# Performance work log

Measured on AMD Instinct MI355X. Metric: run time of the kernel, lower is better.

Reference implementation:

```python
import jax, jax.numpy as jnp
import numpy as np
import jax.scipy.signal as jss

SX, SY, C, K = 256, 256, 3, 10
C0 = [0, 0, 0, 1, 1, 1, 2, 2, 2, 0]
C1 = [[0, 1, 2, 9], [3, 4, 5], [6, 7, 8]]
DD, DT, SIGMA = 5, 0.2, 0.65

_KX = jnp.array([[-1., 0., 1.], [-2., 0., 2.], [-1., 0., 1.]])
_KY = _KX.T


def _conv2(A, Kf):
    # zero-padded 'same' 2D true convolution, vmapped over channel axis
    return jax.vmap(lambda a: jss.convolve2d(a, Kf, mode='same'), in_axes=2, out_axes=2)(A)


def sobel(A):
    # (X, Y, c) -> (X, Y, 2, c): [sobel_y, sobel_x] stacked on axis 2 (FlowLenia convention)
    return jnp.concatenate([_conv2(A, _KY)[:, :, None, :], _conv2(A, _KX)[:, :, None, :]], axis=2)


def growth(U, m, s):
    # bell(U,m,s)*2 - 1
    return jnp.exp(-((U - m) / s) ** 2 / 2.) * 2. - 1.


def get_kernels_fft(R, r, a, w, b):
    # FlowLenia kernel construction: ring distance -> smooth cutoff * sum-of-bumps, normalized, fft2(fftshift)
    mid = SX // 2
    xs = jnp.arange(-mid, mid, dtype=jnp.float32)
    D = jnp.sqrt(xs[:, None] ** 2 + xs[None, :] ** 2)            # (X, Y)
    Dk = D[..., None] / ((R + 15.) * r)                          # (X, Y, k)
    ker = (b * jnp.exp(-(Dk[..., None] - a) ** 2 / w)).sum(-1)   # (X, Y, k)
    sig = 0.5 * (jnp.tanh(-(Dk - 1.) * 10. / 2.) + 1.)           # sigmoid(-(D-1)*10)
    Kk = sig * ker
    nK = Kk / Kk.sum(axis=(0, 1), keepdims=True)
    return jnp.fft.fft2(jnp.fft.fftshift(nK, axes=(0, 1)), axes=(0, 1))


def _rt_apply(A, F):
    # Reintegration tracking with 'wall' border: flow-driven mass redistribution over a (2dd+1)^2 neighborhood
    ii = jnp.arange(SX, dtype=jnp.float32)
    pos = jnp.stack(jnp.meshgrid(ii, ii, indexing='ij'), axis=-1) + 0.5   # (X, Y, 2) cell centers
    ma = DD - SIGMA                                   # max flow magnitude
    mu = pos[..., None] + jnp.clip(DT * F, -ma, ma)   # (X, Y, 2, C) target centers
    mu = jnp.clip(mu, SIGMA, SX - SIGMA)              # wall border
    offs = jnp.arange(-DD, DD + 1)
    gx, gy = jnp.meshgrid(offs, offs, indexing='ij')
    dxs, dys = gx.reshape(-1), gy.reshape(-1)
    clip_hi = min(1., 2. * SIGMA)

    def step(dx, dy):
        Ar = jnp.roll(A, (dx, dy), axis=(0, 1))
        mur = jnp.roll(mu, (dx, dy), axis=(0, 1))
        dpmu = jnp.abs(pos[..., None] - mur)                                  # (X, Y, 2, C)
        sz = 0.5 - dpmu + SIGMA
        area = jnp.prod(jnp.clip(sz, 0., clip_hi), axis=2) / (4. * SIGMA ** 2)  # (X, Y, C)
        return Ar * area

    return jax.vmap(step)(dxs, dys).sum(axis=0)


def setup_inputs() -> dict:
    key = jax.random.key(0)
    ks = jax.random.split(key, 9)
    A = jax.random.uniform(ks[0], (SX, SY, C), dtype=jnp.float32)
    R = jax.random.uniform(ks[1], (), minval=2.0, maxval=25.0)
    r = jax.random.uniform(ks[2], (K,), minval=0.2, maxval=1.0)
    m = jax.random.uniform(ks[3], (K,), minval=0.05, maxval=0.5)
    s = jax.random.uniform(ks[4], (K,), minval=0.001, maxval=0.18)
    h = jax.random.uniform(ks[5], (K,), minval=0.01, maxval=1.0)
    a = jax.random.uniform(ks[6], (K, 3), minval=0.0, maxval=1.0)
    b = jax.random.uniform(ks[7], (K, 3), minval=0.001, maxval=1.0)
    w = jax.random.uniform(ks[8], (K, 3), minval=0.01, maxval=0.5)
    return dict(A=A, R=R, r=r, m=m, s=s, h=h, a=a, b=b, w=w)


def reference(A, R, r, m, s, h, a, b, w):
    fK = get_kernels_fft(R, r, a, w, b)                       # (X, Y, k) complex
    fA = jnp.fft.fft2(A, axes=(0, 1))
    fAk = fA[:, :, jnp.array(C0)]                             # (X, Y, k)
    U = jnp.real(jnp.fft.ifft2(fK * fAk, axes=(0, 1)))        # (X, Y, k)
    U = growth(U, m, s) * h
    U = jnp.dstack([U[:, :, C1[c]].sum(axis=-1) for c in range(C)])  # (X, Y, C)
    nabla_U = sobel(U)                                        # (X, Y, 2, C)
    nabla_A = sobel(A.sum(axis=-1, keepdims=True))            # (X, Y, 2, 1)
    alpha = jnp.clip((A[:, :, None, :] / C) ** 2, 0., 1.)     # (X, Y, 1, C)
    F = nabla_U * (1. - alpha) - nabla_A * alpha              # (X, Y, 2, C)
    return _rt_apply(A, F)
```

## Files before the change

### kernel.cpp

```cpp
#include <hip/hip_runtime.h>

#define NPIX 65536

#define WS_APLANE 0
#define WS_ASUM   (3*NPIX)
#define WS_KOFF   (4*NPIX)
#define WS_MUX    (4*NPIX)
#define WS_MUY    (7*NPIX)
#define WS_UACC   (14*NPIX)
#define WS_ROWS   (24*NPIX)
#define WS_X1RE   (25*NPIX)
#define WS_X1IM   (38*NPIX)
#define WS_X2RE   (51*NPIX)
#define WS_X2IM   (64*NPIX)
#define WS_END    (77*NPIX)

__global__ void k_prep(const float* __restrict__ A,
                       const float* __restrict__ R_, const float* __restrict__ r_,
                       const float* __restrict__ a_, const float* __restrict__ b_,
                       const float* __restrict__ w_, float* __restrict__ ws) {
    int bid = blockIdx.x;
    int t = threadIdx.x;
    if (bid < 256) {
        int idx = bid * 256 + t;
        float a0 = A[idx*3+0], a1 = A[idx*3+1], a2 = A[idx*3+2];
        ws[WS_APLANE + idx]          = a0;
        ws[WS_APLANE + NPIX + idx]   = a1;
        ws[WS_APLANE + 2*NPIX + idx] = a2;
        ws[WS_ASUM + idx] = a0 + a1 + a2;
        return;
    }
    __shared__ float red[4];
    int bk = bid - 256;
    int k = bk >> 8;
    int i = bk & 255;
    int wid = t >> 6, lane = t & 63;
    float R = R_[0];
    float denom = (R + 15.0f) * r_[k];
    int di = i - 128, dj = t - 128;
    float D  = sqrtf((float)(di*di + dj*dj));
    float Dk = D / denom;
    float v = 0.0f;
    if (Dk <= 3.0f) {
        float ker = 0.0f;
        #pragma unroll
        for (int tt = 0; tt < 3; ++tt) {
            float d = Dk - a_[k*3+tt];
            ker += b_[k*3+tt] * expf(-((d*d) / w_[k*3+tt]));
        }
        float sig = 1.0f / (1.0f + expf(10.0f * (Dk - 1.0f)));
        v = sig * ker;
    }
    int iw = (i + 128) & 255;
    int jw = (t + 128) & 255;
    ws[WS_KOFF + k*NPIX + iw*256 + jw] = v;
    float s = v;
    #pragma unroll
    for (int off = 32; off; off >>= 1) s += __shfl_xor(s, off);
    if (lane == 0) red[wid] = s;
    __syncthreads();
    if (t == 0) ws[WS_ROWS + k*256 + i] = red[0] + red[1] + red[2] + red[3];
}

__device__ __forceinline__ void fft256_core(float* __restrict__ re, float* __restrict__ im,
                                            const float* __restrict__ twr,
                                            const float* __restrict__ twi, int lane) {
    #pragma unroll
    for (int s = 1; s <= 8; ++s) {
        int h = 1 << (s - 1);
        #pragma unroll
        for (int b = 0; b < 2; ++b) {
            int idx = b*64 + lane;
            int pos = idx & (h - 1);
            int g   = idx >> (s - 1);
            int i0 = (g << s) + pos;
            int i1 = i0 + h;
            int tj = pos << (8 - s);
            float wr = twr[tj], wi = twi[tj];
            float xr = re[i1], xi = im[i1];
            float br = fmaf(xr, wr, -xi*wi);
            float bi = fmaf(xr, wi,  xi*wr);
            float ar = re[i0], ai = im[i0];
            re[i0] = ar + br; im[i0] = ai + bi;
            re[i1] = ar - br; im[i1] = ai - bi;
        }
    }
}

__device__ __forceinline__ void build_tw(float* twr, float* twi, int t, float sgn) {
    if (t < 128) {
        float ang = (float)t * 0.0245436930f;
        twr[t] = cosf(ang);
        twi[t] = sgn * sinf(ang);
    }
}

__device__ __forceinline__ void store_t4(float* __restrict__ dst, const float* __restrict__ buf,
                                         int off, int t, int lb) {
    float4 v;
    v.x = buf[0*512 + off + t];
    v.y = buf[1*512 + off + t];
    v.z = buf[2*512 + off + t];
    v.w = buf[3*512 + off + t];
    *(float4*)&dst[t*256 + lb] = v;
}

__global__ __launch_bounds__(256) void fft_fwd_packed(float* __restrict__ ws) {
    __shared__ float buf[4*512];
    __shared__ float twr[128], twi[128];
    int p  = blockIdx.x >> 6;
    int lb = (blockIdx.x & 63) * 4;
    int wid = threadIdx.x >> 6, lane = threadIdx.x & 63;
    int t = threadIdx.x;
    build_tw(twr, twi, t, -1.0f);
    int f = 2*p, g = 2*p + 1;
    const float* frow = ws + ((f < 3) ? (WS_APLANE + f*NPIX) : (WS_KOFF + (f-3)*NPIX))
                      + (lb + wid)*256;
    const float* grow = (g < 13)
        ? ws + ((g < 3) ? (WS_APLANE + g*NPIX) : (WS_KOFF + (g-3)*NPIX)) + (lb + wid)*256
        : nullptr;
    float* re = &buf[wid*512];
    float* im = re + 256;
    #pragma unroll
    for (int e = 0; e < 4; ++e) {
        int idx = e*64 + lane;
        int dst = __brev(idx) >> 24;
        re[dst] = frow[idx];
        im[dst] = grow ? grow[idx] : 0.0f;
    }
    __syncthreads();
    fft256_core(re, im, twr, twi, lane);
    __syncthreads();
    int u2 = (256 - t) & 255;
    float4 Fre, Fim, Gre, Gim;
    float* pF[4] = {&Fre.x, &Fim.x, &Gre.x, &Gim.x};
    #pragma unroll
    for (int l = 0; l < 4; ++l) {
        float zr1 = buf[l*512 + t],  zi1 = buf[l*512 + 256 + t];
        float zr2 = buf[l*512 + u2], zi2 = buf[l*512 + 256 + u2];
        pF[0][l] = 0.5f*(zr1 + zr2);
        pF[1][l] = 0.5f*(zi1 - zi2);
        pF[2][l] = 0.5f*(zi1 + zi2);
        pF[3][l] = 0.5f*(zr2 - zr1);
    }
    *(float4*)&ws[WS_X1RE + f*NPIX + t*256 + lb] = Fre;
    *(float4*)&ws[WS_X1IM + f*NPIX + t*256 + lb] = Fim;
    if (g < 13) {
        *(float4*)&ws[WS_X1RE + g*NPIX + t*256 + lb] = Gre;
        *(float4*)&ws[WS_X1IM + g*NPIX + t*256 + lb] = Gim;
    }
}

__global__ __launch_bounds__(256) void fft_fwd_cplx(float* __restrict__ ws) {
    __shared__ float buf[4*512];
    __shared__ float twr[128], twi[128];
    int p  = blockIdx.x >> 6;
    int lb = (blockIdx.x & 63) * 4;
    int wid = threadIdx.x >> 6, lane = threadIdx.x & 63;
    int t = threadIdx.x;
    build_tw(twr, twi, t, -1.0f);
    float* re = &buf[wid*512];
    float* im = re + 256;
    const float* rr = ws + WS_X1RE + p*NPIX + (lb + wid)*256;
    const float* ri = ws + WS_X1IM + p*NPIX + (lb + wid)*256;
    #pragma unroll
    for (int e = 0; e < 4; ++e) {
        int idx = e*64 + lane;
        int dst = __brev(idx) >> 24;
        re[dst] = rr[idx];
        im[dst] = ri[idx];
    }
    __syncthreads();
    fft256_core(re, im, twr, twi, lane);
    __syncthreads();
    store_t4(ws + WS_X2RE + p*NPIX, buf, 0,   t, lb);
    store_t4(ws + WS_X2IM + p*NPIX, buf, 256, t, lb);
}

__global__ __launch_bounds__(256) void ifft_mul_packed(float* __restrict__ ws) {
    __shared__ float buf[4*512];
    __shared__ float twr[128], twi[128];
    int j  = blockIdx.x >> 6;
    int lb = (blockIdx.x & 63) * 4;
    int wid = threadIdx.x >> 6, lane = threadIdx.x & 63;
    int t = threadIdx.x;
    build_tw(twr, twi, t, 1.0f);
    const int C0[10] = {0,0,0,1,1,1,2,2,2,0};
    int ka = 2*j, kb = 2*j + 1;
    int ca = C0[ka], cb = C0[kb];
    int rowoff = (lb + wid)*256;
    const float* arp = ws + WS_X2RE + ca*NPIX + rowoff;
    const float* aip = ws + WS_X2IM + ca*NPIX + rowoff;
    const float* krp = ws + WS_X2RE + (3+ka)*NPIX + rowoff;
    const float* kip = ws + WS_X2IM + (3+ka)*NPIX + rowoff;
    const float* brp = ws + WS_X2RE + cb*NPIX + rowoff;
    const float* bip = ws + WS_X2IM + cb*NPIX + rowoff;
    const float* lrp = ws + WS_X2RE + (3+kb)*NPIX + rowoff;
    const float* lip = ws + WS_X2IM + (3+kb)*NPIX + rowoff;
    float* re = &buf[wid*512];
    float* im = re + 256;
    #pragma unroll
    for (int e = 0; e < 4; ++e) {
        int idx = e*64 + lane;
        int dst = __brev(idx) >> 24;
        float ar = arp[idx], ai = aip[idx];
        float kr = krp[idx], ki = kip[idx];
        float uar = ar*kr - ai*ki;
        float uai = ar*ki + ai*kr;
        float br = brp[idx], bi = bip[idx];
        float lr = lrp[idx], li = lip[idx];
        float ubr = br*lr - bi*li;
        float ubi = br*li + bi*lr;
        re[dst] = uar - ubi;
        im[dst] = uai + ubr;
    }
    __syncthreads();
    fft256_core(re, im, twr, twi, lane);
    __syncthreads();
    store_t4(ws + WS_X1RE + j*NPIX, buf, 0,   t, lb);
    store_t4(ws + WS_X1IM + j*NPIX, buf, 256, t, lb);
}

__global__ __launch_bounds__(256) void ifft_real_packed(float* __restrict__ ws) {
    __shared__ float buf[4*512];
    __shared__ float twr[128], twi[128];
    int j  = blockIdx.x >> 6;
    int lb = (blockIdx.x & 63) * 4;
    int wid = threadIdx.x >> 6, lane = threadIdx.x & 63;
    int t = threadIdx.x;
    build_tw(twr, twi, t, 1.0f);
    float* re = &buf[wid*512];
    float* im = re + 256;
    const float* rr = ws + WS_X1RE + j*NPIX + (lb + wid)*256;
    const float* ri = ws + WS_X1IM + j*NPIX + (lb + wid)*256;
    #pragma unroll
    for (int e = 0; e < 4; ++e) {
        int idx = e*64 + lane;
        int dst = __brev(idx) >> 24;
        re[dst] = rr[idx];
        im[dst] = ri[idx];
    }
    __syncthreads();
    fft256_core(re, im, twr, twi, lane);
    __syncthreads();
    const float sc = 1.0f / 65536.0f;
    float4 va, vb;
    va.x = buf[0*512 + t] * sc;       vb.x = buf[0*512 + 256 + t] * sc;
    va.y = buf[1*512 + t] * sc;       vb.y = buf[1*512 + 256 + t] * sc;
    va.z = buf[2*512 + t] * sc;       vb.z = buf[2*512 + 256 + t] * sc;
    va.w = buf[3*512 + t] * sc;       vb.w = buf[3*512 + 256 + t] * sc;
    *(float4*)&ws[WS_UACC + (2*j)*NPIX   + t*256 + lb] = va;
    *(float4*)&ws[WS_UACC + (2*j+1)*NPIX + t*256 + lb] = vb;
}

__device__ inline void sobel_at(const float* __restrict__ p, int x, int y,
                                float& gy, float& gx) {
    float v[3][3];
    #pragma unroll
    for (int ii = -1; ii <= 1; ++ii)
        #pragma unroll
        for (int jj = -1; jj <= 1; ++jj) {
            int xx = x + ii, yy = y + jj;
            v[ii+1][jj+1] = (xx < 0 || xx > 255 || yy < 0 || yy > 255)
                            ? 0.0f : p[xx*256 + yy];
        }
    gy = (v[0][0] + 2.0f*v[0][1] + v[0][2]) - (v[2][0] + 2.0f*v[2][1] + v[2][2]);
    gx = (v[0][0] + 2.0f*v[1][0] + v[2][0]) - (v[0][2] + 2.0f*v[1][2] + v[2][2]);
}

__global__ __launch_bounds__(256) void growth_mu(float* __restrict__ ws,
                                                 const float* __restrict__ m_,
                                                 const float* __restrict__ s_,
                                                 const float* __restrict__ h_) {
    __shared__ float Ush[3][256];
    __shared__ float kinv[4];
    int b = blockIdx.x;
    int c = b >> 8;
    int x = b & 255;
    int t = threadIdx.x, wid = t >> 6, lane = t & 63;
    int nk = (c == 0) ? 4 : 3;
    if (wid < nk) {
        int k = (wid == 3) ? 9 : c*3 + wid;
        const float* rw = ws + WS_ROWS + k*256;
        float v = rw[lane] + rw[64+lane] + rw[128+lane] + rw[192+lane];
        #pragma unroll
        for (int off = 32; off; off >>= 1) v += __shfl_xor(v, off);
        if (lane == 0) kinv[wid] = 1.0f / v;
    }
    __syncthreads();
    const float* uacc = ws + WS_UACC;
    for (int rr = 0; rr < 3; ++rr) {
        int xr = x - 1 + rr;
        float outv = 0.0f;
        if (xr >= 0 && xr <= 255) {
            int idx = xr*256 + t;
            for (int kk = 0; kk < nk; ++kk) {
                int k = (kk == 3) ? 9 : c*3 + kk;
                float U = uacc[k*NPIX + idx] * kinv[kk];
                float z = (U - m_[k]) / s_[k];
                outv += h_[k] * (expf(-0.5f*z*z)*2.0f - 1.0f);
            }
        }
        Ush[rr][t] = outv;
    }
    __syncthreads();
    int y = t;
    float gyA, gxA;
    sobel_at(ws + WS_ASUM, x, y, gyA, gxA);
    float v[3][3];
    #pragma unroll
    for (int ii = -1; ii <= 1; ++ii)
        #pragma unroll
        for (int jj = -1; jj <= 1; ++jj) {
            int xx = x + ii, yy = y + jj;
            v[ii+1][jj+1] = (xx < 0 || xx > 255 || yy < 0 || yy > 255)
                            ? 0.0f : Ush[ii+1][yy];
        }
    float gy = (v[0][0] + 2.0f*v[0][1] + v[0][2]) - (v[2][0] + 2.0f*v[2][1] + v[2][2]);
    float gx = (v[0][0] + 2.0f*v[1][0] + v[2][0]) - (v[0][2] + 2.0f*v[1][2] + v[2][2]);
    float a = ws[WS_APLANE + c*NPIX + x*256 + y];
    float al = (a / 3.0f); al = al * al;
    al = fminf(fmaxf(al, 0.0f), 1.0f);
    float F0 = gy * (1.0f - al) - gyA * al;
    float F1 = gx * (1.0f - al) - gxA * al;
    float d0 = fminf(fmaxf(0.2f * F0, -4.35f), 4.35f);
    float d1 = fminf(fmaxf(0.2f * F1, -4.35f), 4.35f);
    ws[WS_MUX + c*NPIX + x*256 + y] = fminf(fmaxf((float)x + 0.5f + d0, 0.65f), 255.35f);
    ws[WS_MUY + c*NPIX + x*256 + y] = fminf(fmaxf((float)y + 0.5f + d1, 0.65f), 255.35f);
}

__global__ __launch_bounds__(256) void rt_apply_v2(const float* __restrict__ ws,
                                                   float* __restrict__ out) {
    __shared__ float sA[11*256], sX[11*256], sY[11*256];
    int b = blockIdx.x;
    int c = b >> 8;
    int x = b & 255;
    const float* ap = ws + WS_APLANE + c*NPIX;
    const float* mx = ws + WS_MUX + c*NPIX;
    const float* my = ws + WS_MUY + c*NPIX;
    int t = threadIdx.x;
    #pragma unroll
    for (int i = 0; i < 11; ++i) {
        int src = (((x - (i - 5)) & 255) << 8) + t;
        sA[i*256 + t] = ap[src];
        sX[i*256 + t] = mx[src];
        sY[i*256 + t] = my[src];
    }
    __syncthreads();
    int y = t;
    float px = (float)x + 0.5f, py = (float)y + 0.5f;
    float acc = 0.0f;
    #pragma unroll
    for (int dx = -5; dx <= 5; ++dx) {
        int rb = (dx + 5) * 256;
        for (int dy = -5; dy <= 5; ++dy) {
            int sy = (y - dy) & 255;
            float a  = sA[rb + sy];
            float ax = 1.15f - fabsf(px - sX[rb + sy]);
            float ay = 1.15f - fabsf(py - sY[rb + sy]);
            ax = fminf(fmaxf(ax, 0.0f), 1.0f);
            ay = fminf(fmaxf(ay, 0.0f), 1.0f);
            acc = fmaf(a, ax * ay, acc);
        }
    }
    out[(x*256 + y)*3 + c] = acc * (1.0f / (4.0f * 0.65f * 0.65f));
}

extern "C" void kernel_launch(void* const* d_in, const int* in_sizes, int n_in,
                              void* d_out, int out_size, void* d_ws, size_t ws_size,
                              hipStream_t stream) {
    const float* A = (const float*)d_in[0];
    const float* R = (const float*)d_in[1];
    const float* r = (const float*)d_in[2];
    const float* m = (const float*)d_in[3];
    const float* s = (const float*)d_in[4];
    const float* h = (const float*)d_in[5];
    const float* a = (const float*)d_in[6];
    const float* b = (const float*)d_in[7];
    const float* w = (const float*)d_in[8];
    float* ws  = (float*)d_ws;
    float* out = (float*)d_out;

    k_prep<<<256 + 2560, 256, 0, stream>>>(A, R, r, a, b, w, ws);
    fft_fwd_packed<<<7*64, 256, 0, stream>>>(ws);
    fft_fwd_cplx<<<13*64, 256, 0, stream>>>(ws);
    ifft_mul_packed<<<5*64, 256, 0, stream>>>(ws);
    ifft_real_packed<<<5*64, 256, 0, stream>>>(ws);
    growth_mu<<<768, 256, 0, stream>>>(ws, m, s, h);
    rt_apply_v2<<<768, 256, 0, stream>>>(ws, out);
}
```

Before: 122.5 us.

## Fuse FFT stages and growth/flow with reintegration to cut kernel count

Merges the second forward FFT pass, the spectral multiply and the first inverse pass into one 512-thread kernel per column that keeps all 13 transformed lines in shared memory. The inverse FFT along the other axis reads strided columns directly instead of using transposed stores. Growth, Sobel and mu computation are fused into the reintegration kernel. Each block recomputes mu for 11 rows and growth for 13 rows, trading redundant arithmetic and uncoalesced strided loads for fewer launches and less global round-trip traffic.

Result: slower. 130.2 us (+6.2%).

```diff
diff --git a/kernel.cpp b/kernel.cpp
--- a/kernel.cpp
+++ b/kernel.cpp
@@ -5,62 +5,14 @@
 #define WS_APLANE 0
 #define WS_ASUM   (3*NPIX)
 #define WS_KOFF   (4*NPIX)
-#define WS_MUX    (4*NPIX)
-#define WS_MUY    (7*NPIX)
 #define WS_UACC   (14*NPIX)
 #define WS_ROWS   (24*NPIX)
 #define WS_X1RE   (25*NPIX)
 #define WS_X1IM   (38*NPIX)
-#define WS_X2RE   (51*NPIX)
-#define WS_X2IM   (64*NPIX)
+#define WS_YRE    (51*NPIX)
+#define WS_YIM    (64*NPIX)
 #define WS_END    (77*NPIX)
 
-__global__ void k_prep(const float* __restrict__ A,
-                       const float* __restrict__ R_, const float* __restrict__ r_,
-                       const float* __restrict__ a_, const float* __restrict__ b_,
-                       const float* __restrict__ w_, float* __restrict__ ws) {
-    int bid = blockIdx.x;
-    int t = threadIdx.x;
-    if (bid < 256) {
-        int idx = bid * 256 + t;
-        float a0 = A[idx*3+0], a1 = A[idx*3+1], a2 = A[idx*3+2];
-        ws[WS_APLANE + idx]          = a0;
-        ws[WS_APLANE + NPIX + idx]   = a1;
-        ws[WS_APLANE + 2*NPIX + idx] = a2;
-        ws[WS_ASUM + idx] = a0 + a1 + a2;
-        return;
-    }
-    __shared__ float red[4];
-    int bk = bid - 256;
-    int k = bk >> 8;
-    int i = bk & 255;
-    int wid = t >> 6, lane = t & 63;
-    float R = R_[0];
-    float denom = (R + 15.0f) * r_[k];
-    int di = i - 128, dj = t - 128;
-    float D  = sqrtf((float)(di*di + dj*dj));
-    float Dk = D / denom;
-    float v = 0.0f;
-    if (Dk <= 3.0f) {
-        float ker = 0.0f;
-        #pragma unroll
-        for (int tt = 0; tt < 3; ++tt) {
-            float d = Dk - a_[k*3+tt];
-            ker += b_[k*3+tt] * expf(-((d*d) / w_[k*3+tt]));
-        }
-        float sig = 1.0f / (1.0f + expf(10.0f * (Dk - 1.0f)));
-        v = sig * ker;
-    }
-    int iw = (i + 128) & 255;
-    int jw = (t + 128) & 255;
-    ws[WS_KOFF + k*NPIX + iw*256 + jw] = v;
-    float s = v;
-    #pragma unroll
-    for (int off = 32; off; off >>= 1) s += __shfl_xor(s, off);
-    if (lane == 0) red[wid] = s;
-    __syncthreads();
-    if (t == 0) ws[WS_ROWS + k*256 + i] = red[0] + red[1] + red[2] + red[3];
-}
 
 __device__ __forceinline__ void fft256_core(float* __restrict__ re, float* __restrict__ im,
                                             const float* __restrict__ twr,
@@ -87,48 +39,88 @@
     }
 }
 
-__device__ __forceinline__ void build_tw(float* twr, float* twi, int t, float sgn) {
-    if (t < 128) {
-        float ang = (float)t * 0.0245436930f;
-        twr[t] = cosf(ang);
-        twi[t] = sgn * sinf(ang);
-    }
-}
-
-__device__ __forceinline__ void store_t4(float* __restrict__ dst, const float* __restrict__ buf,
-                                         int off, int t, int lb) {
-    float4 v;
-    v.x = buf[0*512 + off + t];
-    v.y = buf[1*512 + off + t];
-    v.z = buf[2*512 + off + t];
-    v.w = buf[3*512 + off + t];
-    *(float4*)&dst[t*256 + lb] = v;
-}
-
-__global__ __launch_bounds__(256) void fft_fwd_packed(float* __restrict__ ws) {
-    __shared__ float buf[4*512];
+__device__ inline void sobel_at(const float* __restrict__ p, int x, int y,
+                                float& gy, float& gx) {
+    float v[3][3];
+    #pragma unroll
+    for (int ii = -1; ii <= 1; ++ii)
+        #pragma unroll
+        for (int jj = -1; jj <= 1; ++jj) {
+            int xx = x + ii, yy = y + jj;
+            v[ii+1][jj+1] = (xx < 0 || xx > 255 || yy < 0 || yy > 255)
+                            ? 0.0f : p[xx*256 + yy];
+        }
+    gy = (v[0][0] + 2.0f*v[0][1] + v[0][2]) - (v[2][0] + 2.0f*v[2][1] + v[2][2]);
+    gx = (v[0][0] + 2.0f*v[1][0] + v[2][0]) - (v[0][2] + 2.0f*v[1][2] + v[2][2]);
+}
+
+__global__ void k_prep(const float* __restrict__ A, const float* __restrict__ R_,
+                       const float* __restrict__ r_, const float* __restrict__ a_,
+                       const float* __restrict__ b_, const float* __restrict__ w_,
+                       float* __restrict__ ws) {
+    __shared__ float red[4];
+    int u = blockIdx.x;
+    int t = threadIdx.x, wid = t >> 6, lane = t & 63;
+    if (u < 256) {
+        int idx = u*256 + t;
+        float a0 = A[idx*3+0], a1 = A[idx*3+1], a2 = A[idx*3+2];
+        ws[WS_APLANE + idx]          = a0;
+        ws[WS_APLANE + NPIX + idx]   = a1;
+        ws[WS_APLANE + 2*NPIX + idx] = a2;
+        ws[WS_ASUM + idx] = a0 + a1 + a2;
+        return;
+    }
+    int bk = u - 256;
+    int k = bk >> 8, i = bk & 255;
+    float R = R_[0];
+    float denom = (R + 15.0f) * r_[k];
+    int di = i - 128, dj = t - 128;
+    float D  = sqrtf((float)(di*di + dj*dj));
+    float Dk = D / denom;
+    float v = 0.0f;
+    if (Dk <= 3.0f) {
+        float ker = 0.0f;
+        #pragma unroll
+        for (int tt = 0; tt < 3; ++tt) {
+            float d = Dk - a_[k*3+tt];
+            ker += b_[k*3+tt] * expf(-((d*d) / w_[k*3+tt]));
+        }
+        float sig = 1.0f / (1.0f + expf(10.0f * (Dk - 1.0f)));
+        v = sig * ker;
+    }
+    int iw = (i + 128) & 255, jw = (t + 128) & 255;
+    ws[WS_KOFF + k*NPIX + iw*256 + jw] = v;
+    float ssum = v;
+    #pragma unroll
+    for (int off = 32; off; off >>= 1) ssum += __shfl_xor(ssum, off);
+    __syncthreads();
+    if (lane == 0) red[wid] = ssum;
+    __syncthreads();
+    if (t == 0) ws[WS_ROWS + k*256 + i] = red[0]+red[1]+red[2]+red[3];
+}
+
+__global__ __launch_bounds__(256) void k_fft1(float* __restrict__ ws) {
+    __shared__ float buf[2048];
     __shared__ float twr[128], twi[128];
-    int p  = blockIdx.x >> 6;
-    int lb = (blockIdx.x & 63) * 4;
-    int wid = threadIdx.x >> 6, lane = threadIdx.x & 63;
-    int t = threadIdx.x;
-    build_tw(twr, twi, t, -1.0f);
+    int t = threadIdx.x, wid = t >> 6, lane = t & 63;
+    if (t < 128) { float ang = (float)t * 0.0245436930f; twr[t] = cosf(ang); twi[t] = -sinf(ang); }
+    __syncthreads();
+    int p = blockIdx.x >> 6, lb = (blockIdx.x & 63) * 4;
     int f = 2*p, g = 2*p + 1;
     const float* frow = ws + ((f < 3) ? (WS_APLANE + f*NPIX) : (WS_KOFF + (f-3)*NPIX))
                       + (lb + wid)*256;
-    const float* grow = (g < 13)
+    const float* grow_ = (g < 13)
         ? ws + ((g < 3) ? (WS_APLANE + g*NPIX) : (WS_KOFF + (g-3)*NPIX)) + (lb + wid)*256
         : nullptr;
-    float* re = &buf[wid*512];
+    float* re = buf + wid*512;
     float* im = re + 256;
     #pragma unroll
     for (int e = 0; e < 4; ++e) {
         int idx = e*64 + lane;
         int dst = __brev(idx) >> 24;
         re[dst] = frow[idx];
-        im[dst] = grow ? grow[idx] : 0.0f;
-    }
-    __syncthreads();
+        im[dst] = grow_ ? grow_[idx] : 0.0f;
+    }
     fft256_core(re, im, twr, twi, lane);
     __syncthreads();
     int u2 = (256 - t) & 255;
@@ -151,132 +143,119 @@
     }
 }
 
-__global__ __launch_bounds__(256) void fft_fwd_cplx(float* __restrict__ ws) {
+__global__ __launch_bounds__(512) void k_colfft_mul(float* __restrict__ ws) {
+    __shared__ float hat[13*512];
+    __shared__ float pk[5*512];
+    __shared__ float twc[128], twsF[128], twsI[128];
+    int ky = blockIdx.x;
+    int t = threadIdx.x, wave = t >> 6, lane = t & 63;
+    if (t < 128) {
+        float ang = (float)t * 0.0245436930f;
+        twc[t] = cosf(ang);
+        float sv = sinf(ang);
+        twsF[t] = -sv; twsI[t] = sv;
+    }
+    __syncthreads();
+    const int rowbase = ky * 256;
+    #pragma unroll
+    for (int rep = 0; rep < 2; ++rep) {
+        int p = (rep == 0) ? wave : (wave >= 3 ? wave + 5 : 13);
+        if (p < 13) {
+            float* re = &hat[p*512];
+            float* im = re + 256;
+            const float* rr = ws + WS_X1RE + p*NPIX + rowbase;
+            const float* ri = ws + WS_X1IM + p*NPIX + rowbase;
+            #pragma unroll
+            for (int e = 0; e < 4; ++e) {
+                int idx = e*64 + lane;
+                int dst = __brev(idx) >> 24;
+                re[dst] = rr[idx];
+                im[dst] = ri[idx];
+            }
+            fft256_core(re, im, twc, twsF, lane);
+        }
+    }
+    __syncthreads();
+    if (wave < 5) {
+        int j = wave;
+        int ka = 2*j, kb = 2*j + 1;
+        int ca = (ka < 9) ? ka/3 : 0;
+        int cb = (kb < 9) ? kb/3 : 0;
+        const float* Ar = &hat[ca*512];      const float* Ai = Ar + 256;
+        const float* Kr = &hat[(3+ka)*512];  const float* Ki = Kr + 256;
+        const float* Br = &hat[cb*512];      const float* Bi = Br + 256;
+        const float* Lr = &hat[(3+kb)*512];  const float* Li = Lr + 256;
+        float* re = &pk[j*512];
+        float* im = re + 256;
+        #pragma unroll
+        for (int e = 0; e < 4; ++e) {
+            int idx = e*64 + lane;
+            int dst = __brev(idx) >> 24;
+            float ar = Ar[idx], ai = Ai[idx];
+            float kr = Kr[idx], ki = Ki[idx];
+            float uar = ar*kr - ai*ki;
+            float uai = ar*ki + ai*kr;
+            float br = Br[idx], bi = Bi[idx];
+            float lr = Lr[idx], li = Li[idx];
+            float ubr = br*lr - bi*li;
+            float ubi = br*li + bi*lr;
+            re[dst] = uar - ubi;
+            im[dst] = uai + ubr;
+        }
+        fft256_core(re, im, twc, twsI, lane);
+        float* Yre = ws + WS_YRE + j*NPIX + rowbase;
+        float* Yim = ws + WS_YIM + j*NPIX + rowbase;
+        #pragma unroll
+        for (int e = 0; e < 4; ++e) {
+            int idx = e*64 + lane;
+            Yre[idx] = re[idx];
+            Yim[idx] = im[idx];
+        }
+    }
+}
+
+__global__ __launch_bounds__(256) void k_ifft_y(float* __restrict__ ws) {
     __shared__ float buf[4*512];
-    __shared__ float twr[128], twi[128];
-    int p  = blockIdx.x >> 6;
+    __shared__ float twc[128], twsI[128];
+    int t = threadIdx.x, wid = t >> 6, lane = t & 63;
+    if (t < 128) { float ang = (float)t * 0.0245436930f; twc[t] = cosf(ang); twsI[t] = sinf(ang); }
+    __syncthreads();
+    int j  = blockIdx.x >> 6;
     int lb = (blockIdx.x & 63) * 4;
-    int wid = threadIdx.x >> 6, lane = threadIdx.x & 63;
-    int t = threadIdx.x;
-    build_tw(twr, twi, t, -1.0f);
+    int x = lb + wid;
     float* re = &buf[wid*512];
     float* im = re + 256;
-    const float* rr = ws + WS_X1RE + p*NPIX + (lb + wid)*256;
-    const float* ri = ws + WS_X1IM + p*NPIX + (lb + wid)*256;
+    const float* Yre = ws + WS_YRE + j*NPIX + x;
+    const float* Yim = ws + WS_YIM + j*NPIX + x;
     #pragma unroll
     for (int e = 0; e < 4; ++e) {
-        int idx = e*64 + lane;
-        int dst = __brev(idx) >> 24;
-        re[dst] = rr[idx];
-        im[dst] = ri[idx];
-    }
-    __syncthreads();
-    fft256_core(re, im, twr, twi, lane);
-    __syncthreads();
-    store_t4(ws + WS_X2RE + p*NPIX, buf, 0,   t, lb);
-    store_t4(ws + WS_X2IM + p*NPIX, buf, 256, t, lb);
-}
-
-__global__ __launch_bounds__(256) void ifft_mul_packed(float* __restrict__ ws) {
-    __shared__ float buf[4*512];
-    __shared__ float twr[128], twi[128];
-    int j  = blockIdx.x >> 6;
-    int lb = (blockIdx.x & 63) * 4;
-    int wid = threadIdx.x >> 6, lane = threadIdx.x & 63;
-    int t = threadIdx.x;
-    build_tw(twr, twi, t, 1.0f);
-    const int C0[10] = {0,0,0,1,1,1,2,2,2,0};
-    int ka = 2*j, kb = 2*j + 1;
-    int ca = C0[ka], cb = C0[kb];
-    int rowoff = (lb + wid)*256;
-    const float* arp = ws + WS_X2RE + ca*NPIX + rowoff;
-    const float* aip = ws + WS_X2IM + ca*NPIX + rowoff;
-    const float* krp = ws + WS_X2RE + (3+ka)*NPIX + rowoff;
-    const float* kip = ws + WS_X2IM + (3+ka)*NPIX + rowoff;
-    const float* brp = ws + WS_X2RE + cb*NPIX + rowoff;
-    const float* bip = ws + WS_X2IM + cb*NPIX + rowoff;
-    const float* lrp = ws + WS_X2RE + (3+kb)*NPIX + rowoff;
-    const float* lip = ws + WS_X2IM + (3+kb)*NPIX + rowoff;
-    float* re = &buf[wid*512];
-    float* im = re + 256;
+        int ky = e*64 + lane;
+        int dst = __brev(ky) >> 24;
+        re[dst] = Yre[ky*256];
+        im[dst] = Yim[ky*256];
+    }
+    fft256_core(re, im, twc, twsI, lane);
+    const float sc = 1.0f / 65536.0f;
+    float* Ua = ws + WS_UACC + (2*j)*NPIX   + x*256;
+    float* Ub = ws + WS_UACC + (2*j+1)*NPIX + x*256;
     #pragma unroll
     for (int e = 0; e < 4; ++e) {
-        int idx = e*64 + lane;
-        int dst = __brev(idx) >> 24;
-        float ar = arp[idx], ai = aip[idx];
-        float kr = krp[idx], ki = kip[idx];
-        float uar = ar*kr - ai*ki;
-        float uai = ar*ki + ai*kr;
-        float br = brp[idx], bi = bip[idx];
-        float lr = lrp[idx], li = lip[idx];
-        float ubr = br*lr - bi*li;
-        float ubi = br*li + bi*lr;
-        re[dst] = uar - ubi;
-        im[dst] = uai + ubr;
-    }
-    __syncthreads();
-    fft256_core(re, im, twr, twi, lane);
-    __syncthreads();
-    store_t4(ws + WS_X1RE + j*NPIX, buf, 0,   t, lb);
-    store_t4(ws + WS_X1IM + j*NPIX, buf, 256, t, lb);
-}
-
-__global__ __launch_bounds__(256) void ifft_real_packed(float* __restrict__ ws) {
-    __shared__ float buf[4*512];
-    __shared__ float twr[128], twi[128];
-    int j  = blockIdx.x >> 6;
-    int lb = (blockIdx.x & 63) * 4;
-    int wid = threadIdx.x >> 6, lane = threadIdx.x & 63;
-    int t = threadIdx.x;
-    build_tw(twr, twi, t, 1.0f);
-    float* re = &buf[wid*512];
-    float* im = re + 256;
-    const float* rr = ws + WS_X1RE + j*NPIX + (lb + wid)*256;
-    const float* ri = ws + WS_X1IM + j*NPIX + (lb + wid)*256;
-    #pragma unroll
-    for (int e = 0; e < 4; ++e) {
-        int idx = e*64 + lane;
-        int dst = __brev(idx) >> 24;
-        re[dst] = rr[idx];
-        im[dst] = ri[idx];
-    }
-    __syncthreads();
-    fft256_core(re, im, twr, twi, lane);
-    __syncthreads();
-    const float sc = 1.0f / 65536.0f;
-    float4 va, vb;
-    va.x = buf[0*512 + t] * sc;       vb.x = buf[0*512 + 256 + t] * sc;
-    va.y = buf[1*512 + t] * sc;       vb.y = buf[1*512 + 256 + t] * sc;
-    va.z = buf[2*512 + t] * sc;       vb.z = buf[2*512 + 256 + t] * sc;
-    va.w = buf[3*512 + t] * sc;       vb.w = buf[3*512 + 256 + t] * sc;
-    *(float4*)&ws[WS_UACC + (2*j)*NPIX   + t*256 + lb] = va;
-    *(float4*)&ws[WS_UACC + (2*j+1)*NPIX + t*256 + lb] = vb;
-}
-
-__device__ inline void sobel_at(const float* __restrict__ p, int x, int y,
-                                float& gy, float& gx) {
-    float v[3][3];
-    #pragma unroll
-    for (int ii = -1; ii <= 1; ++ii)
-        #pragma unroll
-        for (int jj = -1; jj <= 1; ++jj) {
-            int xx = x + ii, yy = y + jj;
-            v[ii+1][jj+1] = (xx < 0 || xx > 255 || yy < 0 || yy > 255)
-                            ? 0.0f : p[xx*256 + yy];
-        }
-    gy = (v[0][0] + 2.0f*v[0][1] + v[0][2]) - (v[2][0] + 2.0f*v[2][1] + v[2][2]);
-    gx = (v[0][0] + 2.0f*v[1][0] + v[2][0]) - (v[0][2] + 2.0f*v[1][2] + v[2][2]);
-}
-
-__global__ __launch_bounds__(256) void growth_mu(float* __restrict__ ws,
-                                                 const float* __restrict__ m_,
-                                                 const float* __restrict__ s_,
-                                                 const float* __restrict__ h_) {
-    __shared__ float Ush[3][256];
+        int y = e*64 + lane;
+        Ua[y] = re[y] * sc;
+        Ub[y] = im[y] * sc;
+    }
+}
+
+__global__ __launch_bounds__(256) void k_post(float* __restrict__ ws,
+                                              const float* __restrict__ m_,
+                                              const float* __restrict__ s_,
+                                              const float* __restrict__ h_,
+                                              float* __restrict__ out) {
+    __shared__ float sU[13*256];
+    __shared__ float sX[11*256], sY[11*256], sA[11*256];
     __shared__ float kinv[4];
     int b = blockIdx.x;
-    int c = b >> 8;
-    int x = b & 255;
+    int c = b >> 8, x = b & 255;
     int t = threadIdx.x, wid = t >> 6, lane = t & 63;
     int nk = (c == 0) ? 4 : 3;
     if (wid < nk) {
@@ -289,70 +268,53 @@
     }
     __syncthreads();
     const float* uacc = ws + WS_UACC;
-    for (int rr = 0; rr < 3; ++rr) {
-        int xr = x - 1 + rr;
+    for (int rr = 0; rr < 13; ++rr) {
+        int ar = (x - 6 + rr) & 255;
+        int idx = ar*256 + t;
         float outv = 0.0f;
-        if (xr >= 0 && xr <= 255) {
-            int idx = xr*256 + t;
-            for (int kk = 0; kk < nk; ++kk) {
-                int k = (kk == 3) ? 9 : c*3 + kk;
-                float U = uacc[k*NPIX + idx] * kinv[kk];
-                float z = (U - m_[k]) / s_[k];
-                outv += h_[k] * (expf(-0.5f*z*z)*2.0f - 1.0f);
+        for (int kk = 0; kk < nk; ++kk) {
+            int k = (kk == 3) ? 9 : c*3 + kk;
+            float U = uacc[k*NPIX + idx] * kinv[kk];
+            float z = (U - m_[k]) / s_[k];
+            outv += h_[k] * (expf(-0.5f*z*z)*2.0f - 1.0f);
+        }
+        sU[rr*256 + t] = outv;
+    }
+    __syncthreads();
+    int y = t;
+    for (int i = 0; i < 11; ++i) {
+        int w = (x - 5 + i) & 255;
+        float gyA, gxA;
+        sobel_at(ws + WS_ASUM, w, y, gyA, gxA);
+        float v[3][3];
+        #pragma unroll
+        for (int ii = 0; ii < 3; ++ii) {
+            bool zr = (ii == 0 && w == 0) || (ii == 2 && w == 255);
+            #pragma unroll
+            for (int jj = -1; jj <= 1; ++jj) {
+                int yy = y + jj;
+                v[ii][jj+1] = (zr || yy < 0 || yy > 255) ? 0.0f : sU[(i+ii)*256 + yy];
             }
         }
-        Ush[rr][t] = outv;
-    }
-    __syncthreads();
-    int y = t;
-    float gyA, gxA;
-    sobel_at(ws + WS_ASUM, x, y, gyA, gxA);
-    float v[3][3];
-    #pragma unroll
-    for (int ii = -1; ii <= 1; ++ii)
-        #pragma unroll
-        for (int jj = -1; jj <= 1; ++jj) {
-            int xx = x + ii, yy = y + jj;
-            v[ii+1][jj+1] = (xx < 0 || xx > 255 || yy < 0 || yy > 255)
-                            ? 0.0f : Ush[ii+1][yy];
-        }
-    float gy = (v[0][0] + 2.0f*v[0][1] + v[0][2]) - (v[2][0] + 2.0f*v[2][1] + v[2][2]);
-    float gx = (v[0][0] + 2.0f*v[1][0] + v[2][0]) - (v[0][2] + 2.0f*v[1][2] + v[2][2]);
-    float a = ws[WS_APLANE + c*NPIX + x*256 + y];
-    float al = (a / 3.0f); al = al * al;
-    al = fminf(fmaxf(al, 0.0f), 1.0f);
-    float F0 = gy * (1.0f - al) - gyA * al;
-    float F1 = gx * (1.0f - al) - gxA * al;
-    float d0 = fminf(fmaxf(0.2f * F0, -4.35f), 4.35f);
-    float d1 = fminf(fmaxf(0.2f * F1, -4.35f), 4.35f);
-    ws[WS_MUX + c*NPIX + x*256 + y] = fminf(fmaxf((float)x + 0.5f + d0, 0.65f), 255.35f);
-    ws[WS_MUY + c*NPIX + x*256 + y] = fminf(fmaxf((float)y + 0.5f + d1, 0.65f), 255.35f);
-}
-
-__global__ __launch_bounds__(256) void rt_apply_v2(const float* __restrict__ ws,
-                                                   float* __restrict__ out) {
-    __shared__ float sA[11*256], sX[11*256], sY[11*256];
-    int b = blockIdx.x;
-    int c = b >> 8;
-    int x = b & 255;
-    const float* ap = ws + WS_APLANE + c*NPIX;
-    const float* mx = ws + WS_MUX + c*NPIX;
-    const float* my = ws + WS_MUY + c*NPIX;
-    int t = threadIdx.x;
-    #pragma unroll
-    for (int i = 0; i < 11; ++i) {
-        int src = (((x - (i - 5)) & 255) << 8) + t;
-        sA[i*256 + t] = ap[src];
-        sX[i*256 + t] = mx[src];
-        sY[i*256 + t] = my[src];
-    }
-    __syncthreads();
-    int y = t;
+        float gy = (v[0][0] + 2.0f*v[0][1] + v[0][2]) - (v[2][0] + 2.0f*v[2][1] + v[2][2]);
+        float gx = (v[0][0] + 2.0f*v[1][0] + v[2][0]) - (v[0][2] + 2.0f*v[1][2] + v[2][2]);
+        float a = ws[WS_APLANE + c*NPIX + w*256 + y];
+        float al = (a / 3.0f); al = al * al;
+        al = fminf(fmaxf(al, 0.0f), 1.0f);
+        float F0 = gy * (1.0f - al) - gyA * al;
+        float F1 = gx * (1.0f - al) - gxA * al;
+        float d0 = fminf(fmaxf(0.2f * F0, -4.35f), 4.35f);
+        float d1 = fminf(fmaxf(0.2f * F1, -4.35f), 4.35f);
+        sX[i*256 + y] = fminf(fmaxf((float)w + 0.5f + d0, 0.65f), 255.35f);
+        sY[i*256 + y] = fminf(fmaxf((float)y + 0.5f + d1, 0.65f), 255.35f);
+        sA[i*256 + y] = a;
+    }
+    __syncthreads();
     float px = (float)x + 0.5f, py = (float)y + 0.5f;
     float acc = 0.0f;
     #pragma unroll
     for (int dx = -5; dx <= 5; ++dx) {
-        int rb = (dx + 5) * 256;
+        int rb = (5 - dx) * 256;
         for (int dy = -5; dy <= 5; ++dy) {
             int sy = (y - dy) & 255;
             float a  = sA[rb + sy];
@@ -381,11 +343,9 @@
     float* ws  = (float*)d_ws;
     float* out = (float*)d_out;
 
-    k_prep<<<256 + 2560, 256, 0, stream>>>(A, R, r, a, b, w, ws);
-    fft_fwd_packed<<<7*64, 256, 0, stream>>>(ws);
-    fft_fwd_cplx<<<13*64, 256, 0, stream>>>(ws);
-    ifft_mul_packed<<<5*64, 256, 0, stream>>>(ws);
-    ifft_real_packed<<<5*64, 256, 0, stream>>>(ws);
-    growth_mu<<<768, 256, 0, stream>>>(ws, m, s, h);
-    rt_apply_v2<<<768, 256, 0, stream>>>(ws, out);
-}
+    k_prep<<<2816, 256, 0, stream>>>(A, R, r, a, b, w, ws);
+    k_fft1<<<448, 256, 0, stream>>>(ws);
+    k_colfft_mul<<<256, 512, 0, stream>>>(ws);
+    k_ifft_y<<<320, 256, 0, stream>>>(ws);
+    k_post<<<768, 256, 0, stream>>>(ws, m, s, h, out);
+}
```
